# Kernel tuning notes

Hardware: AMD Instinct MI355X
Metric: run time of the kernel (lower is better)

The kernel has to match this reference:

```python
import jax, jax.numpy as jnp
import numpy as np

B, L, DIM, H, HD = 1, 2048, 2048, 16, 128  # head_dim = DIM // H; RoPE pairs = HD // 2


def setup_inputs() -> dict:
    key = jax.random.key(0)
    ks = jax.random.split(key, 6)
    x = jax.random.normal(ks[0], (B, L, DIM), dtype=jnp.float32)
    pe = jax.random.normal(ks[1], (1, 1, L, HD // 2, 2, 2), dtype=jnp.float32)
    qkv_w = jax.random.normal(ks[2], (3 * DIM, DIM), dtype=jnp.float32) * 0.02
    q_scale = jnp.ones((HD,), dtype=jnp.float32)
    k_scale = jnp.ones((HD,), dtype=jnp.float32)
    proj_w = jax.random.normal(ks[3], (DIM, DIM), dtype=jnp.float32) * 0.02
    proj_b = jnp.zeros((DIM,), dtype=jnp.float32)
    return {"x": x, "pe": pe, "qkv_w": qkv_w, "q_scale": q_scale,
            "k_scale": k_scale, "proj_w": proj_w, "proj_b": proj_b}


def _rmsnorm(t, scale):
    # per-head-dim RMSNorm, eps=1e-6, computed in fp32 (inputs already fp32)
    rrms = jax.lax.rsqrt(jnp.mean(t * t, axis=-1, keepdims=True) + 1e-6)
    return t * rrms * scale


def _apply_rope(q, k, pe):
    def rot(t):
        t_ = t.reshape(*t.shape[:-1], -1, 1, 2)  # [B,H,L,HD/2,1,2]
        out = pe[..., 0] * t_[..., 0] + pe[..., 1] * t_[..., 1]  # [B,H,L,HD/2,2]
        return out.reshape(t.shape)
    return rot(q), rot(k)


def reference(x, pe, qkv_w, q_scale, k_scale, proj_w, proj_b):
    b, l, _ = x.shape
    qkv = jnp.einsum('bld,ed->ble', x, qkv_w)  # [B, L, 3*DIM]
    qkv = qkv.reshape(b, l, 3, H, HD)
    # 'B L (K H D) -> K B H L D'
    qkv = jnp.transpose(qkv, (2, 0, 3, 1, 4))
    q, k, v = qkv[0], qkv[1], qkv[2]  # each [B, H, L, HD]
    q = _rmsnorm(q, q_scale)
    k = _rmsnorm(k, k_scale)
    q, k = _apply_rope(q, k, pe)
    scale = 1.0 / jnp.sqrt(jnp.asarray(HD, dtype=q.dtype))
    scores = jnp.einsum('bhqd,bhkd->bhqk', q, k) * scale
    attn = jax.nn.softmax(scores, axis=-1)
    out = jnp.einsum('bhqk,bhkd->bhqd', attn, v)  # [B, H, L, HD]
    out = jnp.transpose(out, (0, 2, 1, 3)).reshape(b, l, H * HD)  # 'B H L D -> B L (H D)'
    return jnp.einsum('bld,ed->ble', out, proj_w) + proj_b
```

## Files before the change

### kernel.cpp

```cpp
#include <hip/hip_runtime.h>
#include <hip/hip_bf16.h>
#include <math.h>

#define L_SEQ 2048
#define DIM   2048
#define NH    16
#define HD    128
#define TDIM  6144

typedef __attribute__((ext_vector_type(8))) short short8;
typedef __attribute__((ext_vector_type(4))) float f32x4;
typedef __attribute__((ext_vector_type(16))) float f32x16;
typedef __attribute__((ext_vector_type(4))) unsigned int u32x4;

__device__ __forceinline__ void gl_lds16(const void* g, void* l) {
  __builtin_amdgcn_global_load_lds(
      (const __attribute__((address_space(1))) unsigned int*)g,
      (__attribute__((address_space(3))) unsigned int*)l, 16, 0, 0);
}

__device__ __forceinline__ short bf16bits(float x) {
  __hip_bfloat16 h = __float2bfloat16(x);
  return *(short*)&h;
}

__device__ __forceinline__ float bits2f(short s) {
  unsigned int u = ((unsigned int)(unsigned short)s) << 16;
  return __uint_as_float(u);
}

__device__ __forceinline__ unsigned int pack_bf16(float a, float b) {
  __hip_bfloat162 h = __float22bfloat162_rn(make_float2(a, b));
  return *(unsigned int*)&h;
}

__global__ __launch_bounds__(256)
void cast2_bf16(const float* __restrict__ a, __hip_bfloat16* __restrict__ oa,
                const float* __restrict__ b, __hip_bfloat16* __restrict__ ob) {
  int i = (blockIdx.x * 256 + threadIdx.x) * 8;
  const float* src;
  __hip_bfloat16* dst;
  int off;
  if (i < DIM * DIM) { src = a; dst = oa; off = i; }
  else               { src = b; dst = ob; off = i - DIM * DIM; }
  float4 v0 = *(const float4*)(src + off);
  float4 v1 = *(const float4*)(src + off + 4);
  short8 o;
  o[0] = bf16bits(v0.x); o[1] = bf16bits(v0.y); o[2] = bf16bits(v0.z); o[3] = bf16bits(v0.w);
  o[4] = bf16bits(v1.x); o[5] = bf16bits(v1.y); o[6] = bf16bits(v1.z); o[7] = bf16bits(v1.w);
  *(short8*)(dst + off) = o;
}

__global__ __launch_bounds__(256)
void cast_bf16(const float* __restrict__ in, __hip_bfloat16* __restrict__ out, int n) {
  int i = (blockIdx.x * 256 + threadIdx.x) * 8;
  if (i >= n) return;
  float4 a = *(const float4*)(in + i);
  float4 b = *(const float4*)(in + i + 4);
  short8 o;
  o[0] = bf16bits(a.x); o[1] = bf16bits(a.y); o[2] = bf16bits(a.z); o[3] = bf16bits(a.w);
  o[4] = bf16bits(b.x); o[5] = bf16bits(b.y); o[6] = bf16bits(b.z); o[7] = bf16bits(b.w);
  *(short8*)(out + i) = o;
}

#define QKV_N 6144
#define QKV_K 2048

__global__ __launch_bounds__(512, 2)
void gemm_qkv_256(const __hip_bfloat16* __restrict__ A,
                  const __hip_bfloat16* __restrict__ B,
                  __hip_bfloat16* __restrict__ C) {
  extern __shared__ char smem[];
  const int tid  = threadIdx.x;
  const int lane = tid & 63, w = tid >> 6;
  const int l15  = lane & 15, quad = lane >> 4;
  const int wm   = w >> 2, wn = w & 3;

  const int orig = blockIdx.x;
  const int c   = orig & 7;
  const int idx = orig >> 3;
  const int by  = (c & 1) * 4 + idx / 6;
  const int bx  = (c >> 1) * 6 + idx % 6;
  const int m0 = by * 256, n0 = bx * 256;

  const int ar0 = tid >> 2,         aq0 = (tid & 3) ^ ((ar0 >> 1) & 3);
  const int ar1 = (512 + tid) >> 2, aq1 = (tid & 3) ^ ((ar1 >> 1) & 3);
  const __hip_bfloat16* pA0 = A + (size_t)(m0 + ar0) * QKV_K + aq0 * 8;
  const __hip_bfloat16* pA1 = A + (size_t)(m0 + ar1) * QKV_K + aq1 * 8;
  const __hip_bfloat16* pB0 = B + (size_t)(n0 + ar0) * QKV_K + aq0 * 8;
  const __hip_bfloat16* pB1 = B + (size_t)(n0 + ar1) * QKV_K + aq1 * 8;
  const int dst0 = w * 1024;

  f32x4 acc[8][4];
#pragma unroll
  for (int mi = 0; mi < 8; ++mi)
#pragma unroll
    for (int ni = 0; ni < 4; ++ni) acc[mi][ni] = (f32x4){0.f, 0.f, 0.f, 0.f};

  const int sq   = (l15 >> 1) & 3;
  const int aoff = ((wm * 128 + l15) * 32 + (quad ^ sq) * 8) * 2;
  const int boff = ((wn * 64 + l15) * 32 + (quad ^ sq) * 8) * 2;

#pragma unroll
  for (int p = 0; p < 3; ++p) {
    char* Sp = smem + p * 32768;
    gl_lds16(pA0 + p * 32, Sp + dst0);
    gl_lds16(pA1 + p * 32, Sp + dst0 + 8192);
    gl_lds16(pB0 + p * 32, Sp + 16384 + dst0);
    gl_lds16(pB1 + p * 32, Sp + 16384 + dst0 + 8192);
  }
  asm volatile("s_waitcnt vmcnt(8)\n\ts_barrier" ::: "memory");

  for (int tb = 0; tb < 64; tb += 4) {
#pragma unroll
    for (int u = 0; u < 4; ++u) {
      const int t  = tb + u;
      const char* As = smem + u * 32768;
      const char* Bs = As + 16384;
      const int tn = (t + 3) & 63;
      char* Sn = smem + ((u + 3) & 3) * 32768;

      short8 a[8];
#pragma unroll
      for (int mi = 0; mi < 8; ++mi)
        a[mi] = *(const short8*)(As + aoff + mi * 1024);
      short8 b0 = *(const short8*)(Bs + boff);
      short8 b1 = *(const short8*)(Bs + boff + 1024);
      gl_lds16(pA0 + tn * 32, Sn + dst0);
      gl_lds16(pA1 + tn * 32, Sn + dst0 + 8192);
      __builtin_amdgcn_s_barrier();
      __builtin_amdgcn_s_setprio(1);
#pragma unroll
      for (int mi = 0; mi < 8; ++mi) {
        acc[mi][0] = __builtin_amdgcn_mfma_f32_16x16x32_bf16(a[mi], b0, acc[mi][0], 0, 0, 0);
        acc[mi][1] = __builtin_amdgcn_mfma_f32_16x16x32_bf16(a[mi], b1, acc[mi][1], 0, 0, 0);
      }
      __builtin_amdgcn_s_setprio(0);
      __builtin_amdgcn_s_barrier();

      short8 b2 = *(const short8*)(Bs + boff + 2048);
      short8 b3 = *(const short8*)(Bs + boff + 3072);
      gl_lds16(pB0 + tn * 32, Sn + 16384 + dst0);
      gl_lds16(pB1 + tn * 32, Sn + 16384 + dst0 + 8192);
      asm volatile("s_waitcnt vmcnt(8)\n\ts_barrier" ::: "memory");
      __builtin_amdgcn_s_setprio(1);
#pragma unroll
      for (int mi = 0; mi < 8; ++mi) {
        acc[mi][2] = __builtin_amdgcn_mfma_f32_16x16x32_bf16(a[mi], b2, acc[mi][2], 0, 0, 0);
        acc[mi][3] = __builtin_amdgcn_mfma_f32_16x16x32_bf16(a[mi], b3, acc[mi][3], 0, 0, 0);
      }
      __builtin_amdgcn_s_setprio(0);
      __builtin_amdgcn_s_barrier();
    }
  }

  const int crow = m0 + wm * 128 + quad * 4;
  const int ccol = n0 + wn * 64 + l15;
#pragma unroll
  for (int mi = 0; mi < 8; ++mi)
#pragma unroll
    for (int ni = 0; ni < 4; ++ni)
#pragma unroll
      for (int r = 0; r < 4; ++r)
        C[(size_t)(crow + mi * 16 + r) * QKV_N + ccol + ni * 16] =
            __float2bfloat16(acc[mi][ni][r]);
}

__global__ __launch_bounds__(256)
void qkv_epilogue(const __hip_bfloat16* __restrict__ C,
                  const float* __restrict__ q_scale, const float* __restrict__ k_scale,
                  const float* __restrict__ pe,
                  __hip_bfloat16* __restrict__ Qb, __hip_bfloat16* __restrict__ Kb,
                  __hip_bfloat16* __restrict__ Vt) {
  const int bid = blockIdx.x;
  const int t = threadIdx.x;
  if (bid < 512) {
    const int sec = bid >> 8;
    const int h   = (bid >> 4) & 15;
    const int rb  = bid & 15;
    const float* scale = sec ? k_scale : q_scale;
    const float qmul = sec ? 1.0f : 0.08838834764831845f;
    __hip_bfloat16* dst = sec ? Kb : Qb;

    const int row = t >> 1, half = t & 1;
    const int l = rb * 128 + row;
    const __hip_bfloat16* grow = C + (size_t)l * TDIM + sec * DIM + h * HD + half * 64;

    float ss = 0.f;
#pragma unroll
    for (int c8 = 0; c8 < 64; c8 += 8) {
      short8 v8 = *(const short8*)(grow + c8);
#pragma unroll
      for (int j = 0; j < 8; ++j) { float f = bits2f(v8[j]); ss += f * f; }
    }
    ss += __shfl_xor(ss, 1);
    const float rrms = rsqrtf(ss * (1.f / 128.f) + 1e-6f);

    const float* perow = pe + (size_t)l * 256 + half * 128;
    __hip_bfloat16* drow = dst + ((size_t)h * L_SEQ + l) * HD + half * 64;

#pragma unroll
    for (int c8 = 0; c8 < 64; c8 += 8) {
      short8 v8 = *(const short8*)(grow + c8);
      float f[8];
#pragma unroll
      for (int j = 0; j < 8; ++j)
        f[j] = bits2f(v8[j]) * rrms * scale[half * 64 + c8 + j];
      short8 o;
#pragma unroll
      for (int p = 0; p < 4; ++p) {
        float4 pp = *(const float4*)(perow + c8 * 2 + p * 4);
        float e = f[2 * p], od = f[2 * p + 1];
        o[2 * p]     = bf16bits((pp.x * e + pp.y * od) * qmul);
        o[2 * p + 1] = bf16bits((pp.z * e + pp.w * od) * qmul);
      }
      *(short8*)(drow + c8) = o;
    }
  } else {
    __shared__ short Tt[128 * 72];
    const int vb = bid - 512;
    const int h = vb >> 5, lb = vb & 31;
    const int l0 = lb * 64;
#pragma unroll
    for (int k = 0; k < 4; ++k) {
      int idx = t + k * 256;
      int row = idx >> 4, c = idx & 15;
      short8 v = *(const short8*)(C + (size_t)(l0 + row) * TDIM + 2 * DIM + h * HD + c * 8);
#pragma unroll
      for (int j = 0; j < 8; ++j) Tt[(c * 8 + j) * 72 + row] = v[j];
    }
    __syncthreads();
    const int d = t >> 1, lh = t & 1;
    __hip_bfloat16* vrow = Vt + ((size_t)h * HD + d) * L_SEQ + l0 + lh * 32;
#pragma unroll
    for (int k = 0; k < 4; ++k) {
      short8 o = *(const short8*)&Tt[d * 72 + lh * 32 + k * 8];
      *(short8*)(vrow + k * 8) = o;
    }
  }
}

#define PJ_N 2048
#define PJ_K 2048

__global__ __launch_bounds__(256, 2)
void gemm_proj_128(const __hip_bfloat16* __restrict__ A,
                   const __hip_bfloat16* __restrict__ B,
                   const float* __restrict__ bias, float* __restrict__ C) {
  __shared__ __align__(16) char smem[65536];
  const int tid  = threadIdx.x;
  const int lane = tid & 63, w = tid >> 6;
  const int l15  = lane & 15, quad = lane >> 4;
  const int wm   = (w >> 1) * 64, wn = (w & 1) * 64;

  const int orig = blockIdx.x;
  const int c   = orig & 7;
  const int idx = orig >> 3;
  const int by  = (c >> 1) * 4 + (idx & 3);
  const int bx  = (c & 1) * 8 + (idx >> 2);
  const int m0 = by * 128, n0 = bx * 128;

  const int ar0 = tid >> 2,         aq0 = (tid & 3) ^ ((ar0 >> 1) & 3);
  const int ar1 = (256 + tid) >> 2, aq1 = (tid & 3) ^ ((ar1 >> 1) & 3);
  const __hip_bfloat16* pA0 = A + (size_t)(m0 + ar0) * PJ_K + aq0 * 8;
  const __hip_bfloat16* pA1 = A + (size_t)(m0 + ar1) * PJ_K + aq1 * 8;
  const __hip_bfloat16* pB0 = B + (size_t)(n0 + ar0) * PJ_K + aq0 * 8;
  const __hip_bfloat16* pB1 = B + (size_t)(n0 + ar1) * PJ_K + aq1 * 8;
  const int dst0 = w * 1024;

  f32x4 acc[4][4];
#pragma unroll
  for (int mi = 0; mi < 4; ++mi)
#pragma unroll
    for (int ni = 0; ni < 4; ++ni) acc[mi][ni] = (f32x4){0.f, 0.f, 0.f, 0.f};

  const int sq   = (l15 >> 1) & 3;
  const int aoff = ((wm + l15) * 32 + (quad ^ sq) * 8) * 2;
  const int boff = 8192 + ((wn + l15) * 32 + (quad ^ sq) * 8) * 2;

#pragma unroll
  for (int p = 0; p < 3; ++p) {
    char* Sp = smem + p * 16384;
    gl_lds16(pA0 + p * 32, Sp + dst0);
    gl_lds16(pA1 + p * 32, Sp + dst0 + 4096);
    gl_lds16(pB0 + p * 32, Sp + 8192 + dst0);
    gl_lds16(pB1 + p * 32, Sp + 8192 + dst0 + 4096);
  }
  asm volatile("s_waitcnt vmcnt(8)\n\ts_barrier" ::: "memory");

  for (int tb = 0; tb < 64; tb += 4) {
#pragma unroll
    for (int u = 0; u < 4; ++u) {
      const int t  = tb + u;
      const char* As = smem + u * 16384;
      const char* Bs = As;
      const int tn = (t + 3) & 63;
      char* Sn = smem + ((u + 3) & 3) * 16384;

      short8 a[4];
#pragma unroll
      for (int mi = 0; mi < 4; ++mi)
        a[mi] = *(const short8*)(As + aoff + mi * 1024);
      short8 b0 = *(const short8*)(Bs + boff);
      short8 b1 = *(const short8*)(Bs + boff + 1024);
      gl_lds16(pA0 + tn * 32, Sn + dst0);
      gl_lds16(pA1 + tn * 32, Sn + dst0 + 4096);
      __builtin_amdgcn_s_barrier();
      __builtin_amdgcn_s_setprio(1);
#pragma unroll
      for (int mi = 0; mi < 4; ++mi) {
        acc[mi][0] = __builtin_amdgcn_mfma_f32_16x16x32_bf16(a[mi], b0, acc[mi][0], 0, 0, 0);
        acc[mi][1] = __builtin_amdgcn_mfma_f32_16x16x32_bf16(a[mi], b1, acc[mi][1], 0, 0, 0);
      }
      __builtin_amdgcn_s_setprio(0);
      __builtin_amdgcn_s_barrier();

      short8 b2 = *(const short8*)(Bs + boff + 2048);
      short8 b3 = *(const short8*)(Bs + boff + 3072);
      gl_lds16(pB0 + tn * 32, Sn + 8192 + dst0);
      gl_lds16(pB1 + tn * 32, Sn + 8192 + dst0 + 4096);
      asm volatile("s_waitcnt vmcnt(8)\n\ts_barrier" ::: "memory");
      __builtin_amdgcn_s_setprio(1);
#pragma unroll
      for (int mi = 0; mi < 4; ++mi) {
        acc[mi][2] = __builtin_amdgcn_mfma_f32_16x16x32_bf16(a[mi], b2, acc[mi][2], 0, 0, 0);
        acc[mi][3] = __builtin_amdgcn_mfma_f32_16x16x32_bf16(a[mi], b3, acc[mi][3], 0, 0, 0);
      }
      __builtin_amdgcn_s_setprio(0);
      __builtin_amdgcn_s_barrier();
    }
  }

  const int crow = m0 + wm + quad * 4;
  const int ccol = n0 + wn + l15;
#pragma unroll
  for (int mi = 0; mi < 4; ++mi)
#pragma unroll
    for (int ni = 0; ni < 4; ++ni) {
      float bv = bias[ccol + ni * 16];
#pragma unroll
      for (int r = 0; r < 4; ++r)
        C[(size_t)(crow + mi * 16 + r) * PJ_N + ccol + ni * 16] =
            acc[mi][ni][r] + bv;
    }
}

#define NZ 4
#define ZLEN (L_SEQ / NZ)

__global__ __launch_bounds__(256, 3)
void attn_mfma(const __hip_bfloat16* __restrict__ Qb,
               const __hip_bfloat16* __restrict__ Kb,
               const __hip_bfloat16* __restrict__ Vt,
               __hip_bfloat16* __restrict__ Opart, float2* __restrict__ ml) {
  const int orig = blockIdx.x;
  const int wg   = (orig & 7) * 128 + (orig >> 3);
  const int h    = wg >> 6;
  const int rem  = wg & 63;
  const int z    = rem >> 4;
  const int q0   = (rem & 15) * 128;
  const int t    = threadIdx.x;
  const int lane = t & 63, w = t >> 6;
  const int l31  = lane & 31;
  const int u    = lane >> 5;

  __shared__ __align__(16) __hip_bfloat16 Ks[64 * 128];
  __shared__ __align__(16) __hip_bfloat16 Vs[128 * 64];

  const __hip_bfloat16* kbase = Kb + (size_t)h * L_SEQ * HD;
  const __hip_bfloat16* vbase = Vt + (size_t)h * HD * L_SEQ;

  short8 aq[8];
  {
    const __hip_bfloat16* qb = Qb + ((size_t)h * L_SEQ + q0 + w * 32 + l31) * HD + u * 8;
#pragma unroll
    for (int hh = 0; hh < 8; ++hh)
      aq[hh] = *(const short8*)(qb + hh * 16);
  }

  f32x16 o[4];
#pragma unroll
  for (int dt = 0; dt < 4; ++dt)
#pragma unroll
    for (int r = 0; r < 16; ++r) o[dt][r] = 0.f;
  float m_run = -1e30f, l_run = 0.f;

  for (int kt = 0; kt < ZLEN / 64; ++kt) {
    const int k0 = z * ZLEN + kt * 64;
#pragma unroll
    for (int i = 0; i < 4; ++i) {
      int krow = w * 16 + i * 4 + (lane >> 4);
      int kch  = (lane & 15) ^ (krow & 7);
      gl_lds16(kbase + (size_t)(k0 + krow) * HD + kch * 8,
               &Ks[(w * 16 + i * 4) * 128]);
    }
#pragma unroll
    for (int i = 0; i < 4; ++i) {
      int vrow = w * 32 + i * 8 + (lane >> 3);
      int vch  = (lane & 7) ^ (vrow & 7);
      gl_lds16(vbase + (size_t)vrow * L_SEQ + k0 + vch * 8,
               &Vs[(w * 32 + i * 8) * 64]);
    }
    __syncthreads();

#pragma unroll
    for (int ks = 0; ks < 2; ++ks) {
      const int krow = ks * 32 + l31;
      const char* krowp = (const char*)Ks + krow * 256;
      const int ksw = krow & 7;
      f32x16 s;
#pragma unroll
      for (int r = 0; r < 16; ++r) s[r] = 0.f;
      __builtin_amdgcn_s_setprio(1);
#pragma unroll
      for (int hh = 0; hh < 8; ++hh) {
        short8 ak = *(const short8*)(krowp + ((hh * 2 + u) ^ ksw) * 16);
        s = __builtin_amdgcn_mfma_f32_32x32x16_bf16(ak, aq[hh], s, 0, 0, 0);
      }
      __builtin_amdgcn_s_setprio(0);

      float rm = s[0];
#pragma unroll
      for (int r = 1; r < 16; ++r) rm = fmaxf(rm, s[r]);
      rm = fmaxf(rm, __shfl_xor(rm, 32));

      if (!__all(rm <= m_run + 8.f)) {
        float mnew = fmaxf(m_run, rm);
        float alpha = __expf(m_run - mnew);
        m_run = mnew;
        l_run *= alpha;
#pragma unroll
        for (int dt = 0; dt < 4; ++dt)
#pragma unroll
          for (int r = 0; r < 16; ++r) o[dt][r] *= alpha;
      }

      float sum = 0.f;
#pragma unroll
      for (int r = 0; r < 16; ++r) {
        float p = __expf(s[r] - m_run);
        s[r] = p;
        sum += p;
      }
      sum += __shfl_xor(sum, 32);
      l_run += sum;

      unsigned int W0 = pack_bf16(s[0],  s[1]),  W1 = pack_bf16(s[2],  s[3]);
      unsigned int W2 = pack_bf16(s[4],  s[5]),  W3 = pack_bf16(s[6],  s[7]);
      unsigned int W4 = pack_bf16(s[8],  s[9]),  W5 = pack_bf16(s[10], s[11]);
      unsigned int W6 = pack_bf16(s[12], s[13]), W7 = pack_bf16(s[14], s[15]);
      asm("v_permlane32_swap_b32 %0, %1" : "+v"(W0), "+v"(W2));
      asm("v_permlane32_swap_b32 %0, %1" : "+v"(W1), "+v"(W3));
      asm("v_permlane32_swap_b32 %0, %1" : "+v"(W4), "+v"(W6));
      asm("v_permlane32_swap_b32 %0, %1" : "+v"(W5), "+v"(W7));
      u32x4 pb0 = {W0, W1, W2, W3};
      u32x4 pb1 = {W4, W5, W6, W7};
      short8 ap0 = *(short8*)&pb0;
      short8 ap1 = *(short8*)&pb1;

      __builtin_amdgcn_s_setprio(1);
#pragma unroll
      for (int dt = 0; dt < 4; ++dt) {
        const int d = dt * 32 + l31;
        const char* vrowp = (const char*)Vs + d * 128;
        const int vsw = d & 7;
        short8 av0 = *(const short8*)(vrowp + ((ks * 4 + u) ^ vsw) * 16);
        o[dt] = __builtin_amdgcn_mfma_f32_32x32x16_bf16(av0, ap0, o[dt], 0, 0, 0);
        short8 av1 = *(const short8*)(vrowp + ((ks * 4 + 2 + u) ^ vsw) * 16);
        o[dt] = __builtin_amdgcn_mfma_f32_32x32x16_bf16(av1, ap1, o[dt], 0, 0, 0);
      }
      __builtin_amdgcn_s_setprio(0);
    }
    __syncthreads();
  }

  const float linv = 1.f / l_run;
  char* Ot = (char*)Ks + w * 8192;
  const int qsw = l31 & 7;
#pragma unroll
  for (int dt = 0; dt < 4; ++dt)
#pragma unroll
    for (int p = 0; p < 8; ++p) {
      unsigned int v = pack_bf16(o[dt][2 * p] * linv, o[dt][2 * p + 1] * linv);
      int dpair = dt * 16 + (p & 1) + (p >> 1) * 4 + 2 * u;
      *(unsigned int*)(Ot + l31 * 256 + ((dpair >> 2) ^ qsw) * 16 + (dpair & 3) * 4) = v;
    }
  __syncthreads();
  {
    const int qr = lane >> 1, half = lane & 1;
    const char* Orow = (char*)Ks + w * 8192 + qr * 256;
    __hip_bfloat16* gout =
        Opart + ((size_t)(z * NH + h) * L_SEQ + q0 + w * 32 + qr) * HD;
#pragma unroll
    for (int c8 = 0; c8 < 8; ++c8) {
      int chunk = half * 8 + c8;
      short8 v = *(const short8*)(Orow + ((chunk ^ (qr & 7)) * 16));
      *(short8*)(gout + chunk * 8) = v;
    }
  }
  if (lane < 32) {
    size_t rb = (size_t)(z * NH + h) * L_SEQ + q0 + w * 32;
    ml[rb + l31] = make_float2(m_run, l_run);
  }
}

__global__ __launch_bounds__(256)
void attn_combine4(const __hip_bfloat16* __restrict__ Opart,
                   const float2* __restrict__ ml,
                   __hip_bfloat16* __restrict__ out) {
  const int h  = blockIdx.y;
  const int q  = blockIdx.x * 16 + (threadIdx.x >> 4);
  const int d8 = (threadIdx.x & 15) * 8;
  size_t idx[NZ];
  float2 a[NZ];
#pragma unroll
  for (int zz = 0; zz < NZ; ++zz) {
    idx[zz] = ((size_t)zz * NH + h) * L_SEQ + q;
    a[zz] = ml[idx[zz]];
  }
  float M = fmaxf(fmaxf(a[0].x, a[1].x), fmaxf(a[2].x, a[3].x));
  float wz[NZ];
  float tot = 0.f;
#pragma unroll
  for (int zz = 0; zz < NZ; ++zz) {
    wz[zz] = __expf(a[zz].x - M) * a[zz].y;
    tot += wz[zz];
  }
  float inv = 1.f / tot;
  float acc[8] = {0.f, 0.f, 0.f, 0.f, 0.f, 0.f, 0.f, 0.f};
#pragma unroll
  for (int zz = 0; zz < NZ; ++zz) {
    short8 ov = *(const short8*)&Opart[idx[zz] * HD + d8];
#pragma unroll
    for (int j = 0; j < 8; ++j) acc[j] += wz[zz] * bits2f(ov[j]);
  }
  short8 r;
#pragma unroll
  for (int j = 0; j < 8; ++j) r[j] = bf16bits(acc[j] * inv);
  *(short8*)&out[(size_t)q * DIM + h * HD + d8] = r;
}

extern "C" void kernel_launch(void* const* d_in, const int* in_sizes, int n_in,
                              void* d_out, int out_size, void* d_ws, size_t ws_size,
                              hipStream_t stream) {
  const float* x       = (const float*)d_in[0];
  const float* pe      = (const float*)d_in[1];
  const float* qkv_w   = (const float*)d_in[2];
  const float* q_scale = (const float*)d_in[3];
  const float* k_scale = (const float*)d_in[4];
  const float* proj_w  = (const float*)d_in[5];
  const float* proj_b  = (const float*)d_in[6];
  float* out = (float*)d_out;

  char* base = (char*)d_ws;
  __hip_bfloat16* xb       = (__hip_bfloat16*)base;
  __hip_bfloat16* wb       = (__hip_bfloat16*)(base + 8388608);
  __hip_bfloat16* Cq       = (__hip_bfloat16*)(base + 33554432);
  __hip_bfloat16* Qb       = (__hip_bfloat16*)base;
  __hip_bfloat16* Kb       = (__hip_bfloat16*)(base + 8388608);
  __hip_bfloat16* Vt       = (__hip_bfloat16*)(base + 16777216);
  __hip_bfloat16* Opart    = (__hip_bfloat16*)(base + 33554432);
  float2*         ml       = (float2*)(base + 25165824);
  __hip_bfloat16* attn_out = (__hip_bfloat16*)base;
  __hip_bfloat16* pwb      = (__hip_bfloat16*)(base + 33554432);

  static bool attr_done = false;
  if (!attr_done) {
    hipFuncSetAttribute((const void*)gemm_qkv_256,
                        hipFuncAttributeMaxDynamicSharedMemorySize, 131072);
    attr_done = true;
  }

  cast2_bf16<<<dim3((DIM * DIM + TDIM * DIM) / (256 * 8)), 256, 0, stream>>>(
      x, xb, qkv_w, wb);

  gemm_qkv_256<<<dim3((TDIM / 256) * (L_SEQ / 256)), 512, 131072, stream>>>(xb, wb, Cq);

  qkv_epilogue<<<dim3(1024), 256, 0, stream>>>(Cq, q_scale, k_scale, pe, Qb, Kb, Vt);

  attn_mfma<<<dim3(NZ * NH * (L_SEQ / 128)), 256, 0, stream>>>(Qb, Kb, Vt, Opart, ml);

  attn_combine4<<<dim3(L_SEQ / 16, NH), 256, 0, stream>>>(Opart, ml, attn_out);

  cast_bf16<<<dim3(DIM * DIM / (256 * 8)), 256, 0, stream>>>(proj_w, pwb, DIM * DIM);

  gemm_proj_128<<<dim3(256), 256, 0, stream>>>(attn_out, pwb, proj_b, out);
}
```

Baseline: 288.7 us.

## Retile QKV GEMM to 256x192 for 256 blocks and fuse proj_w cast

The QKV GEMM tile changes from 256x256 to 256x192, so the grid becomes 256 blocks (one full wave on 256 CUs) instead of 192, and the LDS stage shrinks to 28 KB. The block-to-tile swizzle and the B loads are reworked to match, with only the first four waves loading the second B slab. The proj_w fp32-to-bf16 cast is folded into the first cast kernel, which saves one launch, and the workspace is remapped so ml now lives in the output buffer. In exchange each block does less work per A load, so A traffic rises relative to B.

```diff
diff --git a/kernel.cpp b/kernel.cpp
--- a/kernel.cpp
+++ b/kernel.cpp
@@ -35,32 +35,22 @@
 }
 
 __global__ __launch_bounds__(256)
-void cast2_bf16(const float* __restrict__ a, __hip_bfloat16* __restrict__ oa,
-                const float* __restrict__ b, __hip_bfloat16* __restrict__ ob) {
+void cast3_bf16(const float* __restrict__ a, __hip_bfloat16* __restrict__ oa,
+                const float* __restrict__ b, __hip_bfloat16* __restrict__ ob,
+                const float* __restrict__ c, __hip_bfloat16* __restrict__ oc) {
   int i = (blockIdx.x * 256 + threadIdx.x) * 8;
   const float* src;
   __hip_bfloat16* dst;
   int off;
-  if (i < DIM * DIM) { src = a; dst = oa; off = i; }
-  else               { src = b; dst = ob; off = i - DIM * DIM; }
+  if (i < DIM * DIM)                  { src = a; dst = oa; off = i; }
+  else if (i < DIM * DIM + TDIM * DIM){ src = b; dst = ob; off = i - DIM * DIM; }
+  else                                { src = c; dst = oc; off = i - DIM * DIM - TDIM * DIM; }
   float4 v0 = *(const float4*)(src + off);
   float4 v1 = *(const float4*)(src + off + 4);
   short8 o;
   o[0] = bf16bits(v0.x); o[1] = bf16bits(v0.y); o[2] = bf16bits(v0.z); o[3] = bf16bits(v0.w);
   o[4] = bf16bits(v1.x); o[5] = bf16bits(v1.y); o[6] = bf16bits(v1.z); o[7] = bf16bits(v1.w);
   *(short8*)(dst + off) = o;
-}
-
-__global__ __launch_bounds__(256)
-void cast_bf16(const float* __restrict__ in, __hip_bfloat16* __restrict__ out, int n) {
-  int i = (blockIdx.x * 256 + threadIdx.x) * 8;
-  if (i >= n) return;
-  float4 a = *(const float4*)(in + i);
-  float4 b = *(const float4*)(in + i + 4);
-  short8 o;
-  o[0] = bf16bits(a.x); o[1] = bf16bits(a.y); o[2] = bf16bits(a.z); o[3] = bf16bits(a.w);
-  o[4] = bf16bits(b.x); o[5] = bf16bits(b.y); o[6] = bf16bits(b.z); o[7] = bf16bits(b.w);
-  *(short8*)(out + i) = o;
 }
 
 #define QKV_N 6144
@@ -79,9 +69,9 @@
   const int orig = blockIdx.x;
   const int c   = orig & 7;
   const int idx = orig >> 3;
-  const int by  = (c & 1) * 4 + idx / 6;
-  const int bx  = (c >> 1) * 6 + idx % 6;
-  const int m0 = by * 256, n0 = bx * 256;
+  const int by  = (c >> 2) * 4 + (idx >> 3);
+  const int bx  = (c & 3) * 8 + (idx & 7);
+  const int m0 = by * 256, n0 = bx * 192;
 
   const int ar0 = tid >> 2,         aq0 = (tid & 3) ^ ((ar0 >> 1) & 3);
   const int ar1 = (512 + tid) >> 2, aq1 = (tid & 3) ^ ((ar1 >> 1) & 3);
@@ -91,34 +81,36 @@
   const __hip_bfloat16* pB1 = B + (size_t)(n0 + ar1) * QKV_K + aq1 * 8;
   const int dst0 = w * 1024;
 
-  f32x4 acc[8][4];
+  f32x4 acc[8][3];
 #pragma unroll
   for (int mi = 0; mi < 8; ++mi)
 #pragma unroll
-    for (int ni = 0; ni < 4; ++ni) acc[mi][ni] = (f32x4){0.f, 0.f, 0.f, 0.f};
+    for (int ni = 0; ni < 3; ++ni) acc[mi][ni] = (f32x4){0.f, 0.f, 0.f, 0.f};
 
   const int sq   = (l15 >> 1) & 3;
   const int aoff = ((wm * 128 + l15) * 32 + (quad ^ sq) * 8) * 2;
-  const int boff = ((wn * 64 + l15) * 32 + (quad ^ sq) * 8) * 2;
+  const int boff = 16384 + ((wn * 48 + l15) * 32 + (quad ^ sq) * 8) * 2;
 
 #pragma unroll
   for (int p = 0; p < 3; ++p) {
-    char* Sp = smem + p * 32768;
+    char* Sp = smem + p * 28672;
     gl_lds16(pA0 + p * 32, Sp + dst0);
     gl_lds16(pA1 + p * 32, Sp + dst0 + 8192);
     gl_lds16(pB0 + p * 32, Sp + 16384 + dst0);
-    gl_lds16(pB1 + p * 32, Sp + 16384 + dst0 + 8192);
-  }
-  asm volatile("s_waitcnt vmcnt(8)\n\ts_barrier" ::: "memory");
+    if (w < 4) gl_lds16(pB1 + p * 32, Sp + 24576 + dst0);
+  }
+  if (w < 4) asm volatile("s_waitcnt vmcnt(8)" ::: "memory");
+  else       asm volatile("s_waitcnt vmcnt(6)" ::: "memory");
+  __builtin_amdgcn_s_barrier();
 
   for (int tb = 0; tb < 64; tb += 4) {
 #pragma unroll
     for (int u = 0; u < 4; ++u) {
       const int t  = tb + u;
-      const char* As = smem + u * 32768;
-      const char* Bs = As + 16384;
+      const char* As = smem + (u & 3) * 28672;
+      const char* Bs = As;
       const int tn = (t + 3) & 63;
-      char* Sn = smem + ((u + 3) & 3) * 32768;
+      char* Sn = smem + ((u + 3) & 3) * 28672;
 
       short8 a[8];
 #pragma unroll
@@ -139,27 +131,29 @@
       __builtin_amdgcn_s_barrier();
 
       short8 b2 = *(const short8*)(Bs + boff + 2048);
-      short8 b3 = *(const short8*)(Bs + boff + 3072);
       gl_lds16(pB0 + tn * 32, Sn + 16384 + dst0);
-      gl_lds16(pB1 + tn * 32, Sn + 16384 + dst0 + 8192);
-      asm volatile("s_waitcnt vmcnt(8)\n\ts_barrier" ::: "memory");
+      if (w < 4) {
+        gl_lds16(pB1 + tn * 32, Sn + 24576 + dst0);
+        asm volatile("s_waitcnt vmcnt(8)" ::: "memory");
+      } else {
+        asm volatile("s_waitcnt vmcnt(6)" ::: "memory");
+      }
+      __builtin_amdgcn_s_barrier();
       __builtin_amdgcn_s_setprio(1);
 #pragma unroll
-      for (int mi = 0; mi < 8; ++mi) {
+      for (int mi = 0; mi < 8; ++mi)
         acc[mi][2] = __builtin_amdgcn_mfma_f32_16x16x32_bf16(a[mi], b2, acc[mi][2], 0, 0, 0);
-        acc[mi][3] = __builtin_amdgcn_mfma_f32_16x16x32_bf16(a[mi], b3, acc[mi][3], 0, 0, 0);
-      }
       __builtin_amdgcn_s_setprio(0);
       __builtin_amdgcn_s_barrier();
     }
   }
 
   const int crow = m0 + wm * 128 + quad * 4;
-  const int ccol = n0 + wn * 64 + l15;
+  const int ccol = n0 + wn * 48 + l15;
 #pragma unroll
   for (int mi = 0; mi < 8; ++mi)
 #pragma unroll
-    for (int ni = 0; ni < 4; ++ni)
+    for (int ni = 0; ni < 3; ++ni)
 #pragma unroll
       for (int r = 0; r < 4; ++r)
         C[(size_t)(crow + mi * 16 + r) * QKV_N + ccol + ni * 16] =
@@ -556,13 +550,13 @@
   __hip_bfloat16* xb       = (__hip_bfloat16*)base;
   __hip_bfloat16* wb       = (__hip_bfloat16*)(base + 8388608);
   __hip_bfloat16* Cq       = (__hip_bfloat16*)(base + 33554432);
+  __hip_bfloat16* pwb      = (__hip_bfloat16*)(base + 58720256);
   __hip_bfloat16* Qb       = (__hip_bfloat16*)base;
   __hip_bfloat16* Kb       = (__hip_bfloat16*)(base + 8388608);
   __hip_bfloat16* Vt       = (__hip_bfloat16*)(base + 16777216);
-  __hip_bfloat16* Opart    = (__hip_bfloat16*)(base + 33554432);
-  float2*         ml       = (float2*)(base + 25165824);
+  __hip_bfloat16* Opart    = (__hip_bfloat16*)(base + 25165824);
+  float2*         ml       = (float2*)d_out;
   __hip_bfloat16* attn_out = (__hip_bfloat16*)base;
-  __hip_bfloat16* pwb      = (__hip_bfloat16*)(base + 33554432);
 
   static bool attr_done = false;
   if (!attr_done) {
@@ -571,10 +565,10 @@
     attr_done = true;
   }
 
-  cast2_bf16<<<dim3((DIM * DIM + TDIM * DIM) / (256 * 8)), 256, 0, stream>>>(
-      x, xb, qkv_w, wb);
-
-  gemm_qkv_256<<<dim3((TDIM / 256) * (L_SEQ / 256)), 512, 131072, stream>>>(xb, wb, Cq);
+  cast3_bf16<<<dim3((2 * DIM * DIM + TDIM * DIM) / (256 * 8)), 256, 0, stream>>>(
+      x, xb, qkv_w, wb, proj_w, pwb);
+
+  gemm_qkv_256<<<dim3(256), 512, 114688, stream>>>(xb, wb, Cq);
 
   qkv_epilogue<<<dim3(1024), 256, 0, stream>>>(Cq, q_scale, k_scale, pe, Qb, Kb, Vt);
 
@@ -582,7 +576,5 @@
 
   attn_combine4<<<dim3(L_SEQ / 16, NH), 256, 0, stream>>>(Opart, ml, attn_out);
 
-  cast_bf16<<<dim3(DIM * DIM / (256 * 8)), 256, 0, stream>>>(proj_w, pwb, DIM * DIM);
-
   gemm_proj_128<<<dim3(256), 256, 0, stream>>>(attn_out, pwb, proj_b, out);
 }
```

New measurement: 281.1 us. 2.6% less time.
